# Kernel optimization log

Hardware: AMD Instinct MI355X
Metric: run time of the kernel (lower is better)

The kernel has to match this reference:

```python
import jax, jax.numpy as jnp
import numpy as np

WS = 8         # window size (square)
SHIFT = 4      # shift size
NUM_HEADS = 8

def _layernorm(x, g, b, eps=1e-5):
    m = x.mean(-1, keepdims=True)
    v = ((x - m) ** 2).mean(-1, keepdims=True)
    return (x - m) / jnp.sqrt(v + eps) * g + b

def _rel_index():
    # relative_position_index for num_frames_q = num_frames_kv = 1 (d-term is 0)
    ch = np.arange(WS)
    coords = np.stack(np.meshgrid(ch, ch, indexing='ij'))      # (2, WS, WS)
    flat = coords.reshape(2, -1)                                 # (2, N)
    rel = flat[:, :, None] - flat[:, None, :]                    # (2, N, N)
    idx = (rel[0] + WS - 1) * (2 * WS - 1) + (rel[1] + WS - 1)   # (N, N)
    return jnp.asarray(idx, dtype=jnp.int32)

def setup_inputs() -> dict:
    key = jax.random.key(0)
    ks = jax.random.split(key, 16)
    B, D, H, W, C = 2, 2, 256, 256, 256
    hid = 4 * C
    nW = (H // WS) * (W // WS)
    N = WS * WS
    f = jax.random.normal
    return {
        'x': f(ks[0], (B, D, H, W, C), jnp.float32),
        'mask_matrix': f(ks[1], (nW, N, N), jnp.float32),
        'g1': jnp.ones((C,), jnp.float32),
        'b1': jnp.zeros((C,), jnp.float32),
        'qw': f(ks[2], (C, C), jnp.float32) * 0.02,
        'qb': jnp.zeros((C,), jnp.float32),
        'kvw': f(ks[3], (2 * C, C), jnp.float32) * 0.02,
        'kvb': jnp.zeros((2 * C,), jnp.float32),
        'pw': f(ks[4], (C, C), jnp.float32) * 0.02,
        'pb': jnp.zeros((C,), jnp.float32),
        'bias_table': f(ks[5], ((2 * WS - 1) ** 2, NUM_HEADS), jnp.float32) * 0.02,
        'g2': jnp.ones((C,), jnp.float32),
        'b2': jnp.zeros((C,), jnp.float32),
        'w1': f(ks[6], (hid, C), jnp.float32) * 0.02,
        'bi1': jnp.zeros((hid,), jnp.float32),
        'w2': f(ks[7], (C, hid), jnp.float32) * 0.02,
        'bi2': jnp.zeros((C,), jnp.float32),
    }

def reference(x, mask_matrix, g1, b1, qw, qb, kvw, kvb, pw, pb, bias_table, g2, b2, w1, bi1, w2, bi2):
    B, D, H, W, C = x.shape
    h = NUM_HEADS
    d = C // h
    N = WS * WS
    nH, nWc = H // WS, W // WS
    nwin = nH * nWc

    shortcut = x[:, 0]                       # (B, H, W, C)  (frame 0)
    xn = _layernorm(x, g1, b1)
    xs = jnp.roll(xn, (-SHIFT, -SHIFT), axis=(2, 3))   # cyclic shift

    # window partition: (B, D, H, W, C) -> (B*nwin, D, N, C)
    win = xs.reshape(B, D, nH, WS, nWc, WS, C)
    win = win.transpose(0, 2, 4, 1, 3, 5, 6).reshape(B * nwin, D, N, C)
    q_in = win[:, 0]                          # (B_, N, C) query = frame 0
    kv_in = win[:, 1]                         # (B_, N, C) kv    = frame 1

    q = (q_in @ qw.T + qb).reshape(-1, N, h, d).transpose(0, 2, 1, 3) * (d ** -0.5)
    kv = (kv_in @ kvw.T + kvb).reshape(-1, N, 2, h, d).transpose(2, 0, 3, 1, 4)
    k, v = kv[0], kv[1]                       # (B_, h, N, d)

    attn = jnp.einsum('bhnd,bhmd->bhnm', q, k)            # (B_, h, N, N)
    bias = bias_table[_rel_index()]                        # (N, N, h)
    attn = attn + bias.transpose(2, 0, 1)[None]
    attn = attn.reshape(B, nwin, h, N, N) + mask_matrix[None, :, None]
    attn = jax.nn.softmax(attn.reshape(-1, h, N, N), axis=-1)

    out = jnp.einsum('bhnm,bhmd->bhnd', attn, v)          # (B_, h, N, d)
    out = out.transpose(0, 2, 1, 3).reshape(-1, N, C)
    out = out @ pw.T + pb + q_in                           # residual inside attn

    # window reverse: (B*nwin, N, C) -> (B, H, W, C)
    out = out.reshape(B, nH, nWc, WS, WS, C).transpose(0, 1, 3, 2, 4, 5).reshape(B, H, W, C)
    out = jnp.roll(out, (SHIFT, SHIFT), axis=(1, 2))

    x1 = shortcut + out
    y = _layernorm(x1, g2, b2)
    y = jax.nn.gelu(y @ w1.T + bi1, approximate=False) @ w2.T + bi2
    return x1 + y
```

## Files before the change

### kernel.cpp

```cpp
#include <hip/hip_runtime.h>
#include <hip/hip_bf16.h>
#include <math.h>

#define SHIFT_ 4

typedef __attribute__((ext_vector_type(8))) short bh8;
typedef __attribute__((ext_vector_type(4))) short sh4;
typedef __attribute__((ext_vector_type(4))) float f4;
typedef __attribute__((ext_vector_type(8))) __bf16 bf8t;

static __device__ __forceinline__ f4 mfma16(bh8 a, bh8 b, f4 c){
  return __builtin_amdgcn_mfma_f32_16x16x32_bf16(
    __builtin_bit_cast(bf8t, a), __builtin_bit_cast(bf8t, b), c, 0, 0, 0);
}
static __device__ __forceinline__ unsigned short f2b(float f){
  unsigned u = __builtin_bit_cast(unsigned, f);
  u += 0x7fffu + ((u >> 16) & 1u);
  return (unsigned short)(u >> 16);
}
static __device__ __forceinline__ float b2f(unsigned short h){
  return __builtin_bit_cast(float, ((unsigned)h) << 16);
}
static __device__ __forceinline__ unsigned cvt_pk_bf16(float lo, float hi){
  unsigned r;
  asm("v_cvt_pk_bf16_f32 %0, %1, %2" : "=v"(r) : "v"(lo), "v"(hi));
  return r;
}
static __device__ __forceinline__ float gelu_f(float hv){
  float u = hv * (1.5957691216f + 0.0713548162f * hv * hv);
  return hv * __builtin_amdgcn_rcpf(1.f + __expf(-u));
}

__global__ __launch_bounds__(256) void prep_w(
    const float* __restrict__ qw, const float* __restrict__ kvw,
    const float* __restrict__ pw, const float* __restrict__ w1,
    const float* __restrict__ w2, unsigned short* __restrict__ wb){
  int i = blockIdx.x * 256 + threadIdx.x;
  float v;
  if      (i < 65536)  v = qw[i] * 0.17677669529663687f;
  else if (i < 196608) v = kvw[i - 65536];
  else if (i < 262144) v = pw[i - 196608];
  else if (i < 524288) v = w1[i - 262144];
  else                 v = w2[i - 524288];
  wb[i] = f2b(v);
}

__global__ __launch_bounds__(256) void ln1_win(
    const float* __restrict__ x, const float* __restrict__ g1,
    const float* __restrict__ b1,
    unsigned short* __restrict__ q_in, unsigned short* __restrict__ kv_in){
  int rid  = blockIdx.x * 4 + (threadIdx.x >> 6);
  int lane = threadIdx.x & 63;
  int d    = rid >> 17;
  int rem  = rid & 131071;
  int w = rem >> 6, n = rem & 63;
  int b = w >> 10, hb = (w >> 5) & 31, wbk = w & 31;
  int sh = (hb * 8 + (n >> 3) + SHIFT_) & 255;
  int sw = (wbk * 8 + (n & 7) + SHIFT_) & 255;
  const float* src = x + ((((size_t)(b * 2 + d)) * 256 + sh) * 256 + sw) * 256;
  float4 v = *(const float4*)(src + lane * 4);
  float s  = v.x + v.y + v.z + v.w;
  float ss = v.x * v.x + v.y * v.y + v.z * v.z + v.w * v.w;
  #pragma unroll
  for (int off = 1; off < 64; off <<= 1){ s += __shfl_xor(s, off); ss += __shfl_xor(ss, off); }
  float m    = s * (1.f / 256.f);
  float rstd = rsqrtf(ss * (1.f / 256.f) - m * m + 1e-5f);
  int c = lane * 4;
  float4 g  = *(const float4*)(g1 + c);
  float4 bb = *(const float4*)(b1 + c);
  sh4 o;
  o.x = (short)f2b((v.x - m) * rstd * g.x + bb.x);
  o.y = (short)f2b((v.y - m) * rstd * g.y + bb.y);
  o.z = (short)f2b((v.z - m) * rstd * g.z + bb.z);
  o.w = (short)f2b((v.w - m) * rstd * g.w + bb.w);
  unsigned short* dst = (d == 0 ? q_in : kv_in) + (size_t)rem * 256 + c;
  *(sh4*)dst = o;
}

template<int MODE, int NT>
__global__ __launch_bounds__(512, 4) void gemm_bt(
    const unsigned short* __restrict__ A, const unsigned short* __restrict__ Wt,
    const float* __restrict__ bias, float bias_scale,
    unsigned short* __restrict__ outb, unsigned short* __restrict__ vt,
    float* __restrict__ outf, const unsigned short* __restrict__ qin,
    const float* __restrict__ xsrc){
  __shared__ unsigned short sA[128][64];
  __shared__ unsigned short sB[256][64];
  int m0 = blockIdx.x * 128;
  int tid = threadIdx.x, lane = tid & 63, wid = tid >> 6;
  int wm = wid >> 2, wn = wid & 3;
  int llo = lane & 15, lhi = lane >> 4;
  int lr = lane >> 3, lc = (lane & 7) * 8;
  const f4 FZ = {0.f, 0.f, 0.f, 0.f};
  for (int nt = 0; nt < NT; nt++){
    f4 acc[4][4];
    for (int i = 0; i < 4; i++) for (int j = 0; j < 4; j++) acc[i][j] = FZ;
    for (int t = 0; t < 4; t++){
      int k0 = t * 64;
      #pragma unroll
      for (int c = 0; c < 2; c++){
        int rr = wid * 16 + c * 8;
        __builtin_amdgcn_global_load_lds(
          (const __attribute__((address_space(1))) unsigned int*)(A + (size_t)(m0 + rr + lr) * 256 + k0 + lc),
          (__attribute__((address_space(3))) unsigned int*)&sA[rr][0], 16, 0, 0);
      }
      #pragma unroll
      for (int c = 0; c < 4; c++){
        int rb = wid * 32 + c * 8;
        __builtin_amdgcn_global_load_lds(
          (const __attribute__((address_space(1))) unsigned int*)(Wt + (size_t)(nt * 256 + rb + lr) * 256 + k0 + lc),
          (__attribute__((address_space(3))) unsigned int*)&sB[rb][0], 16, 0, 0);
      }
      __syncthreads();
      #pragma unroll
      for (int ks = 0; ks < 2; ks++){
        bh8 a[4], b[4];
        #pragma unroll
        for (int mi = 0; mi < 4; mi++) a[mi] = *(const bh8*)&sA[wm * 64 + mi * 16 + llo][ks * 32 + lhi * 8];
        #pragma unroll
        for (int nj = 0; nj < 4; nj++) b[nj] = *(const bh8*)&sB[wn * 64 + nj * 16 + llo][ks * 32 + lhi * 8];
        #pragma unroll
        for (int mi = 0; mi < 4; mi++)
          #pragma unroll
          for (int nj = 0; nj < 4; nj++)
            acc[mi][nj] = mfma16(a[mi], b[nj], acc[mi][nj]);
      }
      __syncthreads();
    }
    #pragma unroll
    for (int mi = 0; mi < 4; mi++)
      #pragma unroll
      for (int nj = 0; nj < 4; nj++){
        int col = nt * 256 + wn * 64 + nj * 16 + llo;
        float bv = bias[col] * bias_scale;
        #pragma unroll
        for (int r = 0; r < 4; r++){
          int row = m0 + wm * 64 + mi * 16 + lhi * 4 + r;
          float val = acc[mi][nj][r] + bv;
          if (MODE == 0){
            outb[(size_t)row * 256 + col] = f2b(val);
          } else if (MODE == 1){
            if (col < 256) outb[(size_t)row * 256 + col] = f2b(val);
            else {
              int cv = col - 256, hd = cv >> 5, dd = cv & 31;
              int w = row >> 6, n = row & 63;
              vt[(((size_t)w * 8 + hd) * 32 + dd) * 64 + n] = f2b(val);
            }
          } else {
            int w = row >> 6, n = row & 63;
            int b = w >> 10, hb = (w >> 5) & 31, wbk = w & 31;
            int hh = (hb * 8 + (n >> 3) + SHIFT_) & 255;
            int ww = (wbk * 8 + (n & 7) + SHIFT_) & 255;
            float res = b2f(qin[(size_t)row * 256 + col]);
            float sc  = xsrc[((((size_t)(b * 2)) * 256 + hh) * 256 + ww) * 256 + col];
            outf[(((size_t)b * 256 + hh) * 256 + ww) * 256 + col] = val + res + sc;
          }
        }
      }
  }
}

__global__ __launch_bounds__(64) void attn_k(
    const unsigned short* __restrict__ q, const unsigned short* __restrict__ k,
    const unsigned short* __restrict__ vt, const float* __restrict__ mask,
    const float* __restrict__ bias_table, unsigned short* __restrict__ aout){
  __shared__ unsigned short sQ[64][40];
  __shared__ unsigned short sK[64][40];
  __shared__ unsigned short sVT[32][72];
  __shared__ unsigned short sP[64][72];
  __shared__ float sBias[225];
  int bid = blockIdx.x;
  int w = bid >> 3, hd = bid & 7;
  int lane = threadIdx.x;
  int llo = lane & 15, lhi = lane >> 4;
  for (int i = lane; i < 225; i += 64) sBias[i] = bias_table[i * 8 + hd];
  {
    const unsigned short* qp = q + ((size_t)w * 64 + lane) * 256 + hd * 32;
    const unsigned short* kp = k + ((size_t)w * 64 + lane) * 256 + hd * 32;
    #pragma unroll
    for (int c2 = 0; c2 < 4; c2++){
      *(bh8*)&sQ[lane][c2 * 8] = *(const bh8*)(qp + c2 * 8);
      *(bh8*)&sK[lane][c2 * 8] = *(const bh8*)(kp + c2 * 8);
    }
    const unsigned short* vp = vt + (((size_t)w * 8 + hd) * 32 + (lane >> 1)) * 64 + (lane & 1) * 32;
    #pragma unroll
    for (int c2 = 0; c2 < 4; c2++)
      *(bh8*)&sVT[lane >> 1][(lane & 1) * 32 + c2 * 8] = *(const bh8*)(vp + c2 * 8);
  }
  __syncthreads();
  const f4 FZ = {0.f, 0.f, 0.f, 0.f};
  f4 acc[4][4];
  {
    bh8 a[4], b[4];
    #pragma unroll
    for (int mi = 0; mi < 4; mi++) a[mi] = *(const bh8*)&sQ[mi * 16 + llo][lhi * 8];
    #pragma unroll
    for (int nj = 0; nj < 4; nj++) b[nj] = *(const bh8*)&sK[nj * 16 + llo][lhi * 8];
    #pragma unroll
    for (int mi = 0; mi < 4; mi++)
      #pragma unroll
      for (int nj = 0; nj < 4; nj++)
        acc[mi][nj] = mfma16(a[mi], b[nj], FZ);
  }
  const float* mrow = mask + (size_t)(w & 1023) * 4096;
  #pragma unroll
  for (int mi = 0; mi < 4; mi++){
    #pragma unroll
    for (int r = 0; r < 4; r++){
      int rr = mi * 16 + lhi * 4 + r;
      int yi = rr >> 3, xi = rr & 7;
      float sv[4]; float mx = -1e30f;
      #pragma unroll
      for (int nj = 0; nj < 4; nj++){
        int cc = nj * 16 + llo;
        int idx = (yi - (cc >> 3) + 7) * 15 + (xi - (cc & 7) + 7);
        sv[nj] = acc[mi][nj][r] + sBias[idx] + mrow[rr * 64 + cc];
        mx = fmaxf(mx, sv[nj]);
      }
      #pragma unroll
      for (int off = 1; off < 16; off <<= 1) mx = fmaxf(mx, __shfl_xor(mx, off));
      float sum = 0.f;
      #pragma unroll
      for (int nj = 0; nj < 4; nj++){ sv[nj] = __expf(sv[nj] - mx); sum += sv[nj]; }
      #pragma unroll
      for (int off = 1; off < 16; off <<= 1) sum += __shfl_xor(sum, off);
      float inv = __builtin_amdgcn_rcpf(sum);
      #pragma unroll
      for (int nj = 0; nj < 4; nj++) sP[rr][nj * 16 + llo] = f2b(sv[nj] * inv);
    }
  }
  __syncthreads();
  f4 o[4][2];
  for (int mi = 0; mi < 4; mi++) for (int dj = 0; dj < 2; dj++) o[mi][dj] = FZ;
  #pragma unroll
  for (int ks = 0; ks < 2; ks++){
    bh8 pa[4], vb[2];
    #pragma unroll
    for (int mi = 0; mi < 4; mi++) pa[mi] = *(const bh8*)&sP[mi * 16 + llo][ks * 32 + lhi * 8];
    #pragma unroll
    for (int dj = 0; dj < 2; dj++) vb[dj] = *(const bh8*)&sVT[dj * 16 + llo][ks * 32 + lhi * 8];
    #pragma unroll
    for (int mi = 0; mi < 4; mi++)
      #pragma unroll
      for (int dj = 0; dj < 2; dj++)
        o[mi][dj] = mfma16(pa[mi], vb[dj], o[mi][dj]);
  }
  #pragma unroll
  for (int mi = 0; mi < 4; mi++)
    for (int dj = 0; dj < 2; dj++)
      for (int r = 0; r < 4; r++){
        int rr = mi * 16 + lhi * 4 + r, dd = dj * 16 + llo;
        aout[((size_t)w * 64 + rr) * 256 + hd * 32 + dd] = f2b(o[mi][dj][r]);
      }
}

__global__ __launch_bounds__(256) void ln2_k(
    const float* __restrict__ x1, const float* __restrict__ g2,
    const float* __restrict__ b2, unsigned short* __restrict__ xn){
  int rid  = blockIdx.x * 4 + (threadIdx.x >> 6);
  int lane = threadIdx.x & 63;
  const float* xr = x1 + (size_t)rid * 256;
  float4 v = *(const float4*)(xr + lane * 4);
  float s  = v.x + v.y + v.z + v.w;
  float ss = v.x * v.x + v.y * v.y + v.z * v.z + v.w * v.w;
  #pragma unroll
  for (int off = 1; off < 64; off <<= 1){ s += __shfl_xor(s, off); ss += __shfl_xor(ss, off); }
  float m    = s * (1.f / 256.f);
  float rstd = rsqrtf(ss * (1.f / 256.f) - m * m + 1e-5f);
  int c = lane * 4;
  float4 g  = *(const float4*)(g2 + c);
  float4 bb = *(const float4*)(b2 + c);
  sh4 o;
  o.x = (short)f2b((v.x - m) * rstd * g.x + bb.x);
  o.y = (short)f2b((v.y - m) * rstd * g.y + bb.y);
  o.z = (short)f2b((v.z - m) * rstd * g.z + bb.z);
  o.w = (short)f2b((v.w - m) * rstd * g.w + bb.w);
  *(sh4*)(xn + (size_t)rid * 256 + c) = o;
}

template<int KSTEPS, int EPI, int BIASF>
__global__ __launch_bounds__(256, 3) void mlp_gemm(
    const unsigned short* __restrict__ A, int lda,
    const unsigned short* __restrict__ Bw, int ldb,
    const float* __restrict__ bias,
    unsigned short* __restrict__ outb, int ldo,
    float* __restrict__ outf){
  __shared__ unsigned short sA[128][64];
  __shared__ unsigned short sB[128][64];
  int n0 = blockIdx.x * 128, m0 = blockIdx.y * 128;
  int tid = threadIdx.x, lane = tid & 63, wid = tid >> 6;
  int wm = wid >> 1, wn = wid & 1;
  int llo = lane & 15, lhi = lane >> 4;
  int lr = lane >> 3, lc = (lane & 7) * 8;
  const f4 FZ = {0.f, 0.f, 0.f, 0.f};
  f4 acc[4][4];
  for (int i = 0; i < 4; i++) for (int j = 0; j < 4; j++) acc[i][j] = FZ;

  for (int t = 0; t < KSTEPS; t++){
    int k0 = t * 64;
    #pragma unroll
    for (int c = 0; c < 4; c++){
      int rr = wid * 32 + c * 8 + lr;
      __builtin_amdgcn_global_load_lds(
        (const __attribute__((address_space(1))) unsigned int*)(A + (size_t)(m0 + rr) * lda + k0 + lc),
        (__attribute__((address_space(3))) unsigned int*)&sA[wid * 32 + c * 8][0], 16, 0, 0);
      __builtin_amdgcn_global_load_lds(
        (const __attribute__((address_space(1))) unsigned int*)(Bw + (size_t)(n0 + rr) * ldb + k0 + lc),
        (__attribute__((address_space(3))) unsigned int*)&sB[wid * 32 + c * 8][0], 16, 0, 0);
    }
    __syncthreads();
    #pragma unroll
    for (int ks = 0; ks < 2; ks++){
      bh8 a[4], b[4];
      #pragma unroll
      for (int mi = 0; mi < 4; mi++) a[mi] = *(const bh8*)&sA[wm * 64 + mi * 16 + llo][ks * 32 + lhi * 8];
      #pragma unroll
      for (int nj = 0; nj < 4; nj++) b[nj] = *(const bh8*)&sB[wn * 64 + nj * 16 + llo][ks * 32 + lhi * 8];
      #pragma unroll
      for (int mi = 0; mi < 4; mi++)
        #pragma unroll
        for (int nj = 0; nj < 4; nj++){
          if (EPI == 0) acc[mi][nj] = mfma16(b[nj], a[mi], acc[mi][nj]);
          else          acc[mi][nj] = mfma16(a[mi], b[nj], acc[mi][nj]);
        }
    }
    __syncthreads();
  }
  if (EPI == 0){
    #pragma unroll
    for (int nj = 0; nj < 4; nj++){
      int cb = n0 + wn * 64 + nj * 16 + lhi * 4;
      float4 bv = *(const float4*)(bias + cb);
      #pragma unroll
      for (int mi = 0; mi < 4; mi++){
        int row = m0 + wm * 64 + mi * 16 + llo;
        float g0 = gelu_f(acc[mi][nj][0] + bv.x);
        float g1 = gelu_f(acc[mi][nj][1] + bv.y);
        float g2 = gelu_f(acc[mi][nj][2] + bv.z);
        float g3 = gelu_f(acc[mi][nj][3] + bv.w);
        uint2 p;
        p.x = cvt_pk_bf16(g0, g1);
        p.y = cvt_pk_bf16(g2, g3);
        *(uint2*)(outb + (size_t)row * ldo + cb) = p;
      }
    }
  } else {
    #pragma unroll
    for (int mi = 0; mi < 4; mi++)
      #pragma unroll
      for (int nj = 0; nj < 4; nj++){
        int col = n0 + wn * 64 + nj * 16 + llo;
        float bv = BIASF ? bias[col] : 0.f;
        #pragma unroll
        for (int r = 0; r < 4; r++){
          int row = m0 + wm * 64 + mi * 16 + lhi * 4 + r;
          outf[(size_t)row * 256 + col] += acc[mi][nj][r] + bv;
        }
      }
  }
}

extern "C" void kernel_launch(void* const* d_in, const int* in_sizes, int n_in,
                              void* d_out, int out_size, void* d_ws, size_t ws_size,
                              hipStream_t stream){
  const float* x          = (const float*)d_in[0];
  const float* mask       = (const float*)d_in[1];
  const float* g1         = (const float*)d_in[2];
  const float* b1         = (const float*)d_in[3];
  const float* qw         = (const float*)d_in[4];
  const float* qb         = (const float*)d_in[5];
  const float* kvw        = (const float*)d_in[6];
  const float* kvb        = (const float*)d_in[7];
  const float* pw         = (const float*)d_in[8];
  const float* pb         = (const float*)d_in[9];
  const float* bias_table = (const float*)d_in[10];
  const float* g2         = (const float*)d_in[11];
  const float* b2         = (const float*)d_in[12];
  const float* w1         = (const float*)d_in[13];
  const float* bi1        = (const float*)d_in[14];
  const float* w2         = (const float*)d_in[15];
  const float* bi2        = (const float*)d_in[16];
  float* out = (float*)d_out;
  char* ws = (char*)d_ws;
  const long long MB = 1048576LL;
  unsigned short* wb    = (unsigned short*)(ws);
  unsigned short* q_in  = (unsigned short*)(ws + (long long)(1.5 * MB));
  unsigned short* kv_in = (unsigned short*)(ws + (long long)(65.5 * MB));
  unsigned short* qbuf  = (unsigned short*)(ws + (long long)(129.5 * MB));
  unsigned short* kbuf  = (unsigned short*)(ws + (long long)(193.5 * MB));
  unsigned short* vtb   = (unsigned short*)(ws + (long long)(257.5 * MB));
  unsigned short* aoutb = kv_in;
  unsigned short* xn    = vtb;
  unsigned short* Hh    = q_in;

  prep_w<<<3072, 256, 0, stream>>>(qw, kvw, pw, w1, w2, wb);
  ln1_win<<<65536, 256, 0, stream>>>(x, g1, b1, q_in, kv_in);
  gemm_bt<0, 1><<<1024, 512, 0, stream>>>(q_in, wb, qb, 0.17677669529663687f,
                                          qbuf, nullptr, nullptr, nullptr, nullptr);
  gemm_bt<1, 2><<<1024, 512, 0, stream>>>(kv_in, wb + 65536, kvb, 1.0f,
                                          kbuf, vtb, nullptr, nullptr, nullptr);
  attn_k<<<16384, 64, 0, stream>>>(qbuf, kbuf, vtb, mask, bias_table, aoutb);
  gemm_bt<2, 1><<<1024, 512, 0, stream>>>(aoutb, wb + 196608, pb, 1.0f,
                                          nullptr, nullptr, out, q_in, x);
  ln2_k<<<32768, 256, 0, stream>>>(out, g2, b2, xn);
  const unsigned short* w1b = wb + 262144;
  const unsigned short* w2b = wb + 524288;
  for (int h = 0; h < 2; h++){
    const long long R = (long long)h * 65536;
    mlp_gemm<4, 0, 0><<<dim3(8, 512), 256, 0, stream>>>(xn + R * 256, 256, w1b, 256,
                                                        bi1, Hh, 1024, nullptr);
    mlp_gemm<16, 1, 1><<<dim3(2, 512), 256, 0, stream>>>(Hh, 1024, w2b, 1024,
                                                         bi2, nullptr, 0, out + R * 256);
  }
}
```

Baseline: 887.8 us.

## Vectorize Q/KV GEMM epilogue stores and transpose V inside attention kernel

For the Q and KV projection GEMMs, the MFMA operands are swapped so each lane holds four consecutive output columns. The epilogue then writes packed 8-byte bf16 stores instead of scattered 2-byte ones. V is now written row-major instead of as a strided transposed layout. The attention kernel loads V row-major and transposes it through LDS, moving the strided-store cost out of the GEMM in exchange for extra LDS work and shared memory per attention block.

After: 829.1 us. 1.07x faster.

```diff
diff --git a/kernel.cpp b/kernel.cpp
--- a/kernel.cpp
+++ b/kernel.cpp
@@ -81,7 +81,7 @@
 __global__ __launch_bounds__(512, 4) void gemm_bt(
     const unsigned short* __restrict__ A, const unsigned short* __restrict__ Wt,
     const float* __restrict__ bias, float bias_scale,
-    unsigned short* __restrict__ outb, unsigned short* __restrict__ vt,
+    unsigned short* __restrict__ outb, unsigned short* __restrict__ vpl,
     float* __restrict__ outf, const unsigned short* __restrict__ qin,
     const float* __restrict__ xsrc){
   __shared__ unsigned short sA[128][64];
@@ -122,50 +122,63 @@
         #pragma unroll
         for (int mi = 0; mi < 4; mi++)
           #pragma unroll
-          for (int nj = 0; nj < 4; nj++)
-            acc[mi][nj] = mfma16(a[mi], b[nj], acc[mi][nj]);
+          for (int nj = 0; nj < 4; nj++){
+            if (MODE < 2) acc[mi][nj] = mfma16(b[nj], a[mi], acc[mi][nj]);
+            else          acc[mi][nj] = mfma16(a[mi], b[nj], acc[mi][nj]);
+          }
       }
       __syncthreads();
     }
-    #pragma unroll
-    for (int mi = 0; mi < 4; mi++)
+    if (MODE < 2){
       #pragma unroll
       for (int nj = 0; nj < 4; nj++){
-        int col = nt * 256 + wn * 64 + nj * 16 + llo;
-        float bv = bias[col] * bias_scale;
-        #pragma unroll
-        for (int r = 0; r < 4; r++){
-          int row = m0 + wm * 64 + mi * 16 + lhi * 4 + r;
-          float val = acc[mi][nj][r] + bv;
-          if (MODE == 0){
-            outb[(size_t)row * 256 + col] = f2b(val);
-          } else if (MODE == 1){
-            if (col < 256) outb[(size_t)row * 256 + col] = f2b(val);
-            else {
-              int cv = col - 256, hd = cv >> 5, dd = cv & 31;
-              int w = row >> 6, n = row & 63;
-              vt[(((size_t)w * 8 + hd) * 32 + dd) * 64 + n] = f2b(val);
-            }
-          } else {
+        int cb = wn * 64 + nj * 16 + lhi * 4;
+        int col = nt * 256 + cb;
+        float4 bv = *(const float4*)(bias + col);
+        #pragma unroll
+        for (int mi = 0; mi < 4; mi++){
+          int row = m0 + wm * 64 + mi * 16 + llo;
+          float f0 = acc[mi][nj][0] + bv.x * bias_scale;
+          float f1 = acc[mi][nj][1] + bv.y * bias_scale;
+          float f2 = acc[mi][nj][2] + bv.z * bias_scale;
+          float f3 = acc[mi][nj][3] + bv.w * bias_scale;
+          uint2 p;
+          p.x = cvt_pk_bf16(f0, f1);
+          p.y = cvt_pk_bf16(f2, f3);
+          if (MODE == 0 || nt == 0) *(uint2*)(outb + (size_t)row * 256 + cb) = p;
+          else                      *(uint2*)(vpl  + (size_t)row * 256 + cb) = p;
+        }
+      }
+    } else {
+      #pragma unroll
+      for (int mi = 0; mi < 4; mi++)
+        #pragma unroll
+        for (int nj = 0; nj < 4; nj++){
+          int col = wn * 64 + nj * 16 + llo;
+          float bv = bias[col] * bias_scale;
+          #pragma unroll
+          for (int r = 0; r < 4; r++){
+            int row = m0 + wm * 64 + mi * 16 + lhi * 4 + r;
             int w = row >> 6, n = row & 63;
             int b = w >> 10, hb = (w >> 5) & 31, wbk = w & 31;
             int hh = (hb * 8 + (n >> 3) + SHIFT_) & 255;
             int ww = (wbk * 8 + (n & 7) + SHIFT_) & 255;
             float res = b2f(qin[(size_t)row * 256 + col]);
             float sc  = xsrc[((((size_t)(b * 2)) * 256 + hh) * 256 + ww) * 256 + col];
-            outf[(((size_t)b * 256 + hh) * 256 + ww) * 256 + col] = val + res + sc;
+            outf[(((size_t)b * 256 + hh) * 256 + ww) * 256 + col] = acc[mi][nj][r] + bv + res + sc;
           }
         }
-      }
+    }
   }
 }
 
 __global__ __launch_bounds__(64) void attn_k(
     const unsigned short* __restrict__ q, const unsigned short* __restrict__ k,
-    const unsigned short* __restrict__ vt, const float* __restrict__ mask,
+    const unsigned short* __restrict__ v, const float* __restrict__ mask,
     const float* __restrict__ bias_table, unsigned short* __restrict__ aout){
   __shared__ unsigned short sQ[64][40];
   __shared__ unsigned short sK[64][40];
+  __shared__ unsigned short sV[64][34];
   __shared__ unsigned short sVT[32][72];
   __shared__ unsigned short sP[64][72];
   __shared__ float sBias[225];
@@ -177,15 +190,13 @@
   {
     const unsigned short* qp = q + ((size_t)w * 64 + lane) * 256 + hd * 32;
     const unsigned short* kp = k + ((size_t)w * 64 + lane) * 256 + hd * 32;
+    const unsigned short* vp = v + ((size_t)w * 64 + lane) * 256 + hd * 32;
     #pragma unroll
     for (int c2 = 0; c2 < 4; c2++){
       *(bh8*)&sQ[lane][c2 * 8] = *(const bh8*)(qp + c2 * 8);
       *(bh8*)&sK[lane][c2 * 8] = *(const bh8*)(kp + c2 * 8);
-    }
-    const unsigned short* vp = vt + (((size_t)w * 8 + hd) * 32 + (lane >> 1)) * 64 + (lane & 1) * 32;
-    #pragma unroll
-    for (int c2 = 0; c2 < 4; c2++)
-      *(bh8*)&sVT[lane >> 1][(lane & 1) * 32 + c2 * 8] = *(const bh8*)(vp + c2 * 8);
+      *(bh8*)&sV[lane][c2 * 8] = *(const bh8*)(vp + c2 * 8);
+    }
   }
   __syncthreads();
   const f4 FZ = {0.f, 0.f, 0.f, 0.f};
@@ -201,6 +212,14 @@
       #pragma unroll
       for (int nj = 0; nj < 4; nj++)
         acc[mi][nj] = mfma16(a[mi], b[nj], FZ);
+  }
+  {
+    int dv = lane >> 1, n0 = (lane & 1) * 32;
+    #pragma unroll
+    for (int i = 0; i < 32; i += 2){
+      unsigned lo = sV[n0 + i][dv], hi = sV[n0 + i + 1][dv];
+      *(unsigned*)&sVT[dv][n0 + i] = lo | (hi << 16);
+    }
   }
   const float* mrow = mask + (size_t)(w & 1023) * 4096;
   #pragma unroll
@@ -388,9 +407,9 @@
   unsigned short* kv_in = (unsigned short*)(ws + (long long)(65.5 * MB));
   unsigned short* qbuf  = (unsigned short*)(ws + (long long)(129.5 * MB));
   unsigned short* kbuf  = (unsigned short*)(ws + (long long)(193.5 * MB));
-  unsigned short* vtb   = (unsigned short*)(ws + (long long)(257.5 * MB));
+  unsigned short* vbuf  = (unsigned short*)(ws + (long long)(257.5 * MB));
   unsigned short* aoutb = kv_in;
-  unsigned short* xn    = vtb;
+  unsigned short* xn    = vbuf;
   unsigned short* Hh    = q_in;
 
   prep_w<<<3072, 256, 0, stream>>>(qw, kvw, pw, w1, w2, wb);
@@ -398,8 +417,8 @@
   gemm_bt<0, 1><<<1024, 512, 0, stream>>>(q_in, wb, qb, 0.17677669529663687f,
                                           qbuf, nullptr, nullptr, nullptr, nullptr);
   gemm_bt<1, 2><<<1024, 512, 0, stream>>>(kv_in, wb + 65536, kvb, 1.0f,
-                                          kbuf, vtb, nullptr, nullptr, nullptr);
-  attn_k<<<16384, 64, 0, stream>>>(qbuf, kbuf, vtb, mask, bias_table, aoutb);
+                                          kbuf, vbuf, nullptr, nullptr, nullptr);
+  attn_k<<<16384, 64, 0, stream>>>(qbuf, kbuf, vbuf, mask, bias_table, aoutb);
   gemm_bt<2, 1><<<1024, 512, 0, stream>>>(aoutb, wb + 196608, pb, 1.0f,
                                           nullptr, nullptr, out, q_in, x);
   ln2_k<<<32768, 256, 0, stream>>>(out, g2, b2, xn);
```
